# Performance work log

Measured on AMD Instinct MI355X. Metric: run time of the kernel, lower is better.

## Reference

```python
import jax, jax.numpy as jnp
import numpy as np

N_HEAD = 16
N_EMBD = 1024
BLOCK = 2048
B, T = 4, 2048


def setup_inputs() -> dict:
    key = jax.random.key(0)
    ks = jax.random.split(key, 5)
    scale = 1.0 / np.sqrt(N_EMBD)
    return {
        "x": jax.random.normal(ks[0], (B, T, N_EMBD), dtype=jnp.float32),
        "W_attn": jax.random.normal(ks[1], (N_EMBD, 3 * N_EMBD), dtype=jnp.float32) * scale,
        "b_attn": jax.random.normal(ks[2], (3 * N_EMBD,), dtype=jnp.float32) * 0.02,
        "W_proj": jax.random.normal(ks[3], (N_EMBD, N_EMBD), dtype=jnp.float32) * scale,
        "b_proj": jax.random.normal(ks[4], (N_EMBD,), dtype=jnp.float32) * 0.02,
    }


def reference(x, W_attn, b_attn, W_proj, b_proj):
    Bb, Tt, C = x.shape
    hd = C // N_HEAD
    qkv = x @ W_attn + b_attn                      # [B,T,3C]
    q, k, v = jnp.split(qkv, 3, axis=2)
    # [B,H,T,hd]
    q = q.reshape(Bb, Tt, N_HEAD, hd).transpose(0, 2, 1, 3)
    k = k.reshape(Bb, Tt, N_HEAD, hd).transpose(0, 2, 1, 3)
    v = v.reshape(Bb, Tt, N_HEAD, hd).transpose(0, 2, 1, 3)
    att = jnp.einsum('bhqd,bhkd->bhqk', q, k) / np.sqrt(hd).astype(x.dtype)
    causal = jnp.tril(jnp.ones((Tt, Tt), dtype=bool))
    att = jnp.where(causal[None, None], att, jnp.finfo(att.dtype).min)
    att = jax.nn.softmax(att, axis=-1)
    y = jnp.einsum('bhqk,bhkd->bhqd', att, v)      # [B,H,T,hd]
    y = y.transpose(0, 2, 1, 3).reshape(Bb, Tt, C)
    return y @ W_proj + b_proj
```

## Files before the change

kernel.cpp:

```cpp
#include <hip/hip_runtime.h>
#include <stdint.h>

typedef unsigned short u16;
typedef __bf16 bf16;
typedef bf16 bf16x8 __attribute__((ext_vector_type(8)));
typedef float f32x4 __attribute__((ext_vector_type(4)));
typedef u16 u16x8 __attribute__((ext_vector_type(8)));
typedef u16 u16x4 __attribute__((ext_vector_type(4)));

#define T_SEQ 2048
#define NHEAD 16
#define HD    64
#define CEMB  1024
#define QS    8388608
#define QSCALE 0.18033688011112042f

__device__ __forceinline__ u16 f2b(float f){
  bf16 h = (bf16)f;
  return __builtin_bit_cast(u16, h);
}
__device__ __forceinline__ void glds16(const void* g, const void* l){
  __builtin_amdgcn_global_load_lds(
    (__attribute__((address_space(1))) unsigned int*)(uintptr_t)g,
    (__attribute__((address_space(3))) unsigned int*)(uintptr_t)l,
    16, 0, 0);
}

__global__ __launch_bounds__(256) void prep_kernel(
    const float* __restrict__ x, u16* __restrict__ xb,
    const float* __restrict__ Wa, u16* __restrict__ Wta,
    const float* __restrict__ Wp, u16* __restrict__ Wtp)
{
  __shared__ __align__(16) u16 tile[64][72];
  const int bid = blockIdx.x;
  const int tid = threadIdx.x;
  if (bid < 4096){
    const int i = (bid * 256 + tid) * 8;
    f32x4 a = *(const f32x4*)&x[i];
    f32x4 b = *(const f32x4*)&x[i + 4];
    u16x8 h;
    #pragma unroll
    for (int j = 0; j < 4; j++){ h[j] = f2b(a[j]); h[4+j] = f2b(b[j]); }
    *(u16x8*)&xb[i] = h;
    return;
  }
  const float* src; u16* dst; int K, N, bx, by;
  if (bid < 4864){ const int j = bid - 4096; src = Wa; dst = Wta; K = 1024; N = 3072; bx = j % 48; by = j / 48; }
  else           { const int j = bid - 4864; src = Wp; dst = Wtp; K = 1024; N = 1024; bx = j % 16; by = j / 16; }
  const int n0 = bx * 64, k0 = by * 64;
  #pragma unroll
  for (int it = 0; it < 4; it++){
    const int idx = it * 256 + tid;
    const int row = idx >> 4, c4 = (idx & 15) * 4;
    f32x4 v = *(const f32x4*)&src[(size_t)(k0 + row) * N + n0 + c4];
    #pragma unroll
    for (int j = 0; j < 4; j++) tile[row][c4 + j] = f2b(v[j]);
  }
  __syncthreads();
  const int r = tid >> 3, cc = (tid & 7) * 8;
  #pragma unroll
  for (int i = 0; i < 2; i++){
    const int rr = r + i * 32;
    u16x8 v;
    #pragma unroll
    for (int j = 0; j < 8; j++) v[j] = tile[cc + j][rr];
    *(u16x8*)&dst[(size_t)(n0 + rr) * K + k0 + cc] = v;
  }
}

template<int MODE>
__global__ __launch_bounds__(256) void gemm_bt(
    const u16* __restrict__ A, const u16* __restrict__ Bt,
    const float* __restrict__ bias, void* __restrict__ outraw, int Ktot)
{
  __shared__ __align__(16) u16 As[128*64];
  __shared__ __align__(16) u16 Bs[128*64];
  const int tid = threadIdx.x;
  const int lane = tid & 63, wave = tid >> 6;
  const int l15 = lane & 15, l4 = lane >> 4;
  const int wm = wave >> 1, wn = wave & 1;
  const int m0 = blockIdx.y * 128, n0 = blockIdx.x * 128;

  f32x4 acc[4][4] = {};

  for (int k0 = 0; k0 < Ktot; k0 += 64){
    #pragma unroll
    for (int ii = 0; ii < 4; ii++){
      const int slot0 = (wave*4 + ii) * 64;
      const int s = slot0 + lane;
      const int row = s >> 3;
      const int c = (s & 7) ^ (row & 7);
      glds16(&A [(size_t)(m0 + row) * Ktot + k0 + c*8], &As[slot0*8]);
      glds16(&Bt[(size_t)(n0 + row) * Ktot + k0 + c*8], &Bs[slot0*8]);
    }
    __syncthreads();
    #pragma unroll
    for (int ks = 0; ks < 2; ks++){
      bf16x8 af[4], bfr[4];
      #pragma unroll
      for (int mt = 0; mt < 4; mt++){
        const int rf = wm*64 + mt*16 + l15;
        const int slot = rf*8 + ((ks*4 + l4) ^ (rf & 7));
        af[mt] = *(const bf16x8*)&As[slot*8];
      }
      #pragma unroll
      for (int nt = 0; nt < 4; nt++){
        const int rf = wn*64 + nt*16 + l15;
        const int slot = rf*8 + ((ks*4 + l4) ^ (rf & 7));
        bfr[nt] = *(const bf16x8*)&Bs[slot*8];
      }
      #pragma unroll
      for (int mt = 0; mt < 4; mt++)
        #pragma unroll
        for (int nt = 0; nt < 4; nt++)
          acc[mt][nt] = __builtin_amdgcn_mfma_f32_16x16x32_bf16(
              af[mt], bfr[nt], acc[mt][nt], 0, 0, 0);
    }
    __syncthreads();
  }

  #pragma unroll
  for (int nt = 0; nt < 4; nt++){
    const int n = n0 + wn*64 + nt*16 + l15;
    const float bias_v = bias[n];
    if (MODE == 0){
      u16* out = (u16*)outraw;
      const int which = n >> 10;
      const int cc = n & 1023;
      const int h = cc >> 6, d = cc & 63;
      const float sc = (which == 0) ? QSCALE : 1.0f;
      if (which == 2){
        #pragma unroll
        for (int mt = 0; mt < 4; mt++){
          const int rowg = m0 + wm*64 + mt*16 + l4*4;
          const int bb = rowg >> 11, t = rowg & 2047;
          u16x4 pk;
          #pragma unroll
          for (int r = 0; r < 4; r++) pk[r] = f2b(acc[mt][nt][r] + bias_v);
          *(u16x4*)&out[(size_t)2*QS + ((size_t)(bb*NHEAD + h)*HD + d)*T_SEQ + t] = pk;
        }
      } else {
        #pragma unroll
        for (int mt = 0; mt < 4; mt++)
          #pragma unroll
          for (int r = 0; r < 4; r++){
            const int rowg = m0 + wm*64 + mt*16 + l4*4 + r;
            const int bb = rowg >> 11, t = rowg & 2047;
            out[(size_t)which*QS + ((size_t)(bb*NHEAD + h)*T_SEQ + t)*HD + d]
                = f2b((acc[mt][nt][r] + bias_v) * sc);
          }
      }
    } else {
      float* out = (float*)outraw;
      #pragma unroll
      for (int mt = 0; mt < 4; mt++)
        #pragma unroll
        for (int r = 0; r < 4; r++){
          const int rowg = m0 + wm*64 + mt*16 + l4*4 + r;
          out[(size_t)rowg*CEMB + n] = acc[mt][nt][r] + bias_v;
        }
    }
  }
}

__global__ __launch_bounds__(256, 4) void attn_kernel(
    const u16* __restrict__ qb, const u16* __restrict__ kb,
    const u16* __restrict__ vtb, u16* __restrict__ y)
{
  __shared__ __align__(16) u16 Ks[64*64];
  __shared__ __align__(16) u16 Vt[64*64];
  __shared__ __align__(16) u16 Pw[8*16*72];
  const int tid = threadIdx.x;
  const int lane = tid & 63, wave = tid >> 6;
  const int l15 = lane & 15, l4 = lane >> 4;
  const int qt = 15 - (blockIdx.x >> 6);
  const int bh = blockIdx.x & 63;
  const int q0 = qt * 128;
  const size_t base = (size_t)bh * (T_SEQ * HD);
  const u16* qp  = qb  + base;
  const u16* kp  = kb  + base;
  const u16* vtp = vtb + base;

  const int qmin0 = q0 + wave*32;
  const int qmin1 = qmin0 + 16;

  bf16x8 qf[2][2];
  #pragma unroll
  for (int g = 0; g < 2; g++){
    const int m = qmin0 + g*16 + l15;
    qf[g][0] = *(const bf16x8*)&qp[m*HD +      l4*8];
    qf[g][1] = *(const bf16x8*)&qp[m*HD + 32 + l4*8];
  }
  f32x4 o[2][4] = {};
  float l_run[2] = {0.f, 0.f};

  const int s0i = (wave*2 + 0) * 64 + lane;
  const int s1i = (wave*2 + 1) * 64 + lane;
  const int row0 = s0i >> 3, c0 = (s0i & 7) ^ (row0 & 7);
  const int row1 = s1i >> 3, c1 = (s1i & 7) ^ (row1 & 7);
  const int koff0 = row0*HD + c0*8, koff1 = row1*HD + c1*8;
  const int voff0 = row0*T_SEQ + c0*8, voff1 = row1*T_SEQ + c1*8;
  const int ldso0 = (wave*2 + 0) * 64 * 8, ldso1 = (wave*2 + 1) * 64 * 8;

  const int nkt = 2*qt + 2;
  for (int kt = 0; kt < nkt; kt++){
    __syncthreads();
    glds16(&kp [kt*4096 + koff0], &Ks[ldso0]);
    glds16(&kp [kt*4096 + koff1], &Ks[ldso1]);
    glds16(&vtp[kt*64   + voff0], &Vt[ldso0]);
    glds16(&vtp[kt*64   + voff1], &Vt[ldso1]);
    __syncthreads();

    const int t0 = kt*64;
    if (t0 <= qmin1 + 15){
      const bool act0 = (t0 <= qmin0 + 15);

      f32x4 s0[4], s1[4];
      #pragma unroll
      for (int nb = 0; nb < 4; nb++){
        f32x4 a0 = {}, a1 = {};
        #pragma unroll
        for (int ks = 0; ks < 2; ks++){
          const int rf = nb*16 + l15;
          const int slot = rf*8 + ((ks*4 + l4) ^ (rf & 7));
          bf16x8 kf = *(const bf16x8*)&Ks[slot*8];
          a1 = __builtin_amdgcn_mfma_f32_16x16x32_bf16(kf, qf[1][ks], a1, 0, 0, 0);
          if (act0)
            a0 = __builtin_amdgcn_mfma_f32_16x16x32_bf16(kf, qf[0][ks], a0, 0, 0, 0);
        }
        s1[nb] = a1; s0[nb] = a0;
      }

      #pragma unroll
      for (int g = 0; g < 2; g++){
        if (g == 0 && !act0) continue;
        f32x4* sf = (g == 0) ? s0 : s1;
        const int qmin = (g == 0) ? qmin0 : qmin1;
        const int qg = qmin + l15;
        float lsum = 0.f;
        if (t0 + 63 > qmin){
          #pragma unroll
          for (int nb = 0; nb < 4; nb++){
            u16x4 pk;
            #pragma unroll
            for (int r = 0; r < 4; r++){
              const int t = t0 + nb*16 + l4*4 + r;
              float p = __builtin_amdgcn_exp2f(sf[nb][r]);
              p = (t <= qg) ? p : 0.0f;
              lsum += p;
              pk[r] = f2b(p);
            }
            *(u16x4*)&Pw[(wave*2 + g)*1152 + l15*72 + nb*16 + l4*4] = pk;
          }
        } else {
          #pragma unroll
          for (int nb = 0; nb < 4; nb++){
            u16x4 pk;
            #pragma unroll
            for (int r = 0; r < 4; r++){
              const float p = __builtin_amdgcn_exp2f(sf[nb][r]);
              lsum += p;
              pk[r] = f2b(p);
            }
            *(u16x4*)&Pw[(wave*2 + g)*1152 + l15*72 + nb*16 + l4*4] = pk;
          }
        }
        l_run[g] += lsum;
      }

      #pragma unroll
      for (int ks = 0; ks < 2; ks++){
        bf16x8 pf1 = *(const bf16x8*)&Pw[(wave*2 + 1)*1152 + l15*72 + ks*32 + l4*8];
        bf16x8 pf0;
        if (act0) pf0 = *(const bf16x8*)&Pw[(wave*2 + 0)*1152 + l15*72 + ks*32 + l4*8];
        #pragma unroll
        for (int nh = 0; nh < 4; nh++){
          const int rf = nh*16 + l15;
          const int slot = rf*8 + ((ks*4 + l4) ^ (rf & 7));
          bf16x8 vf = *(const bf16x8*)&Vt[slot*8];
          o[1][nh] = __builtin_amdgcn_mfma_f32_16x16x32_bf16(vf, pf1, o[1][nh], 0, 0, 0);
          if (act0)
            o[0][nh] = __builtin_amdgcn_mfma_f32_16x16x32_bf16(vf, pf0, o[0][nh], 0, 0, 0);
        }
      }
    }
  }

  const int b = bh >> 4, h = bh & 15;
  #pragma unroll
  for (int g = 0; g < 2; g++){
    float lr = l_run[g];
    lr += __shfl_xor(lr, 16);
    lr += __shfl_xor(lr, 32);
    const float inv_l = 1.0f / lr;
    const int t = qmin0 + g*16 + l15;
    #pragma unroll
    for (int nh = 0; nh < 4; nh++){
      u16x4 pk;
      #pragma unroll
      for (int r = 0; r < 4; r++) pk[r] = f2b(o[g][nh][r] * inv_l);
      *(u16x4*)&y[((size_t)(b*T_SEQ + t))*CEMB + h*HD + nh*16 + l4*4] = pk;
    }
  }
}

extern "C" void kernel_launch(void* const* d_in, const int* in_sizes, int n_in,
                              void* d_out, int out_size, void* d_ws, size_t ws_size,
                              hipStream_t stream) {
  const float* x      = (const float*)d_in[0];
  const float* W_attn = (const float*)d_in[1];
  const float* b_attn = (const float*)d_in[2];
  const float* W_proj = (const float*)d_in[3];
  const float* b_proj = (const float*)d_in[4];
  float* out = (float*)d_out;
  u16* ws  = (u16*)d_ws;

  u16* Wt_attn = ws;
  u16* Wt_proj = ws + 3145728;
  u16* xb      = ws + 4194304;
  u16* qkv     = ws + 12582912;
  u16* y       = xb;

  prep_kernel<<<5120, 256, 0, stream>>>(x, xb, W_attn, Wt_attn, W_proj, Wt_proj);
  gemm_bt<0><<<dim3(24, 64), 256, 0, stream>>>(xb, Wt_attn, b_attn, qkv, 1024);
  attn_kernel<<<1024, 256, 0, stream>>>(qkv, qkv + QS, qkv + 2*QS, y);
  gemm_bt<1><<<dim3(8, 64), 256, 0, stream>>>(y, Wt_proj, b_proj, out, 1024);
}
```

Baseline: 241.3 us.

## Prefetch next K/V tile into registers instead of direct global-to-LDS loads

Replaces the synchronous global_load_lds copies of the K and V^T tiles with register prefetching. The next tile is loaded into registers while the current tile is being computed, then stored to LDS at the top of the next iteration. This is meant to hide global-memory latency behind the MFMA work. In exchange it uses more registers and adds explicit LDS store instructions.

```diff
diff --git a/kernel.cpp b/kernel.cpp
--- a/kernel.cpp
+++ b/kernel.cpp
@@ -194,22 +194,31 @@
   f32x4 o[2][4] = {};
   float l_run[2] = {0.f, 0.f};
 
-  const int s0i = (wave*2 + 0) * 64 + lane;
-  const int s1i = (wave*2 + 1) * 64 + lane;
-  const int row0 = s0i >> 3, c0 = (s0i & 7) ^ (row0 & 7);
-  const int row1 = s1i >> 3, c1 = (s1i & 7) ^ (row1 & 7);
-  const int koff0 = row0*HD + c0*8, koff1 = row1*HD + c1*8;
-  const int voff0 = row0*T_SEQ + c0*8, voff1 = row1*T_SEQ + c1*8;
-  const int ldso0 = (wave*2 + 0) * 64 * 8, ldso1 = (wave*2 + 1) * 64 * 8;
+  const int sA = tid, sB = tid + 256;
+  const int rowA = sA >> 3, cA = (sA & 7) ^ (rowA & 7);
+  const int rowB = sB >> 3, cB = (sB & 7) ^ (rowB & 7);
+  const int koffA = rowA*HD + cA*8, koffB = rowB*HD + cB*8;
+  const int voffA = rowA*T_SEQ + cA*8, voffB = rowB*T_SEQ + cB*8;
+
+  u16x8 kra = *(const u16x8*)&kp [koffA];
+  u16x8 krb = *(const u16x8*)&kp [koffB];
+  u16x8 vra = *(const u16x8*)&vtp[voffA];
+  u16x8 vrb = *(const u16x8*)&vtp[voffB];
 
   const int nkt = 2*qt + 2;
   for (int kt = 0; kt < nkt; kt++){
     __syncthreads();
-    glds16(&kp [kt*4096 + koff0], &Ks[ldso0]);
-    glds16(&kp [kt*4096 + koff1], &Ks[ldso1]);
-    glds16(&vtp[kt*64   + voff0], &Vt[ldso0]);
-    glds16(&vtp[kt*64   + voff1], &Vt[ldso1]);
+    *(u16x8*)&Ks[sA*8] = kra;
+    *(u16x8*)&Ks[sB*8] = krb;
+    *(u16x8*)&Vt[sA*8] = vra;
+    *(u16x8*)&Vt[sB*8] = vrb;
     __syncthreads();
+    if (kt + 1 < nkt){
+      kra = *(const u16x8*)&kp [(kt+1)*4096 + koffA];
+      krb = *(const u16x8*)&kp [(kt+1)*4096 + koffB];
+      vra = *(const u16x8*)&vtp[(kt+1)*64   + voffA];
+      vrb = *(const u16x8*)&vtp[(kt+1)*64   + voffB];
+    }
 
     const int t0 = kt*64;
     if (t0 <= qmin1 + 15){
```

Result: slower. 273.6 us (+13.4%).
